# Performance work log

Measured on AMD Instinct MI355X. Metric: run time of the kernel, lower is better.

Reference implementation:

```python
import jax, jax.numpy as jnp
import numpy as np
from jax import lax

B, C_IN, C_OUT, K, STYLE_DIM, H, W = 16, 128, 128, 3, 512, 128, 128
EPS = 1e-8


def setup_inputs() -> dict:
    key = jax.random.key(0)
    k1, k2, k3, k4 = jax.random.split(key, 4)
    x = jax.random.normal(k1, (B, C_IN, H, W), dtype=jnp.float32)
    style_vector = jax.random.normal(k2, (B, STYLE_DIM), dtype=jnp.float32)
    # EqualizedLR(nn.Linear(style_dim, in_channels)): weight ~ N(0,1), bias = 0
    proj_w = jax.random.normal(k3, (C_IN, STYLE_DIM), dtype=jnp.float32)
    proj_b = jnp.zeros((C_IN,), dtype=jnp.float32)
    # base conv weight (1, out, in, k, k) ~ N(0,1)
    weight = jax.random.normal(k4, (1, C_OUT, C_IN, K, K), dtype=jnp.float32)
    return {"x": x, "style_vector": style_vector, "proj_w": proj_w,
            "proj_b": proj_b, "weight": weight}


def reference(x, style_vector, proj_w, proj_b, weight):
    b = x.shape[0]
    # EqualizedLR: scale input by gain / sqrt(fan_in), gain=1, fan_in=style_dim
    scale = 1.0 / jnp.sqrt(jnp.float32(STYLE_DIM))
    style = (style_vector * scale) @ proj_w.T + proj_b          # [b, in]
    # modulate: [1,out,in,k,k] * [b,1,in,1,1] -> [b,out,in,k,k]
    w = weight * style[:, None, :, None, None]
    # demodulate
    demod = lax.rsqrt(jnp.sum(w * w, axis=(2, 3, 4)) + EPS)     # [b, out]
    w = w * demod[:, :, None, None, None]
    # grouped conv with groups=b == per-sample conv; vmap over batch
    pad = K // 2
    def conv_one(xi, wi):
        # xi: [in,H,W], wi: [out,in,k,k]
        return lax.conv_general_dilated(
            xi[None], wi, window_strides=(1, 1),
            padding=[(pad, pad), (pad, pad)],
            dimension_numbers=("NCHW", "OIHW", "NCHW"))[0]
    out = jax.vmap(conv_one)(x, w)                               # [b,out,H,W]
    return out
```

## Files before the change

kernel.cpp:

```cpp
#include <hip/hip_runtime.h>
#include <cstdint>

#define B_   16
#define CIN  128
#define COUT 128
#define SD   512
#define H_   128
#define W_   128

typedef __bf16 bf16x8  __attribute__((ext_vector_type(8)));
typedef float  floatx4 __attribute__((ext_vector_type(4)));
typedef float floatx16 __attribute__((ext_vector_type(16)));

__global__ void style_kernel(const float* __restrict__ sv, const float* __restrict__ pw,
                             const float* __restrict__ pb, float* __restrict__ style) {
    int bid = blockIdx.x;
    int b = bid >> 7, c = bid & 127;
    int lane = threadIdx.x;
    const float* svb = sv + b * SD;
    const float* pwc = pw + (size_t)c * SD;
    float s = 0.f;
#pragma unroll
    for (int i = 0; i < SD; i += 64) s += svb[i + lane] * pwc[i + lane];
#pragma unroll
    for (int off = 32; off > 0; off >>= 1) s += __shfl_down(s, off, 64);
    if (lane == 0) style[b * CIN + c] = s * 0.044194173824159216f + pb[c];
}

__global__ void modw_kernel(const float* __restrict__ weight, const float* __restrict__ style,
                            __bf16* __restrict__ wmod) {
    int bid = blockIdx.x;
    int b = bid >> 7, o = bid & 127;
    int c = threadIdx.x;
    float s = style[b * CIN + c];
    const float* wp = weight + ((size_t)o * CIN + c) * 9;
    float v[9];
    float ss = 0.f;
#pragma unroll
    for (int t = 0; t < 9; ++t) { v[t] = wp[t] * s; ss += v[t] * v[t]; }
#pragma unroll
    for (int off = 32; off > 0; off >>= 1) ss += __shfl_down(ss, off, 64);
    __shared__ float sh[2];
    int wid = c >> 6, lane = c & 63;
    if (lane == 0) sh[wid] = ss;
    __syncthreads();
    float d = rsqrtf(sh[0] + sh[1] + 1e-8f);
    int chunk = c >> 4, ci = c & 15;
#pragma unroll
    for (int t = 0; t < 9; ++t) {
        wmod[(((((size_t)b * 9 + t) * 8 + chunk) * 128 + o) * 16 + ci)] = (__bf16)(v[t] * d);
    }
}

__global__ __launch_bounds__(256)
void xpose_kernel(const float* __restrict__ x, __bf16* __restrict__ xT) {
    int ch = blockIdx.x;
    int hq = blockIdx.y;
    int b  = blockIdx.z;
    int t  = threadIdx.x;
    int wq = t & 31;
    int cp = t >> 5;
    int c0 = ch * 16 + cp * 2;
    const float* xa = x + (((size_t)b * CIN + c0    ) * H_ + hq * 8) * W_ + wq * 4;
    const float* xc = x + (((size_t)b * CIN + c0 + 1) * H_ + hq * 8) * W_ + wq * 4;
    uint32_t* dst = (uint32_t*)xT + ((((size_t)b * 8 + ch) * H_ + hq * 8) * W_) * 8 + cp;
#pragma unroll
    for (int hr = 0; hr < 8; ++hr) {
        floatx4 a  = *(const floatx4*)(xa + (size_t)hr * W_);
        floatx4 b2 = *(const floatx4*)(xc + (size_t)hr * W_);
#pragma unroll
        for (int j = 0; j < 4; ++j) {
            unsigned short lo = __builtin_bit_cast(unsigned short, (__bf16)a[j]);
            unsigned short hi = __builtin_bit_cast(unsigned short, (__bf16)b2[j]);
            dst[(size_t)hr * W_ * 8 + (size_t)(wq * 4 + j) * 8] =
                (uint32_t)lo | ((uint32_t)hi << 16);
        }
    }
}

#define WXT 66
__global__ __launch_bounds__(256, 4)
void conv_kernel(const __bf16* __restrict__ xT, const __bf16* __restrict__ wmod,
                 float* __restrict__ out) {
    __shared__ __align__(16) __bf16 Xs[4 * WXT * 16];
    int w0 = blockIdx.x * 64;
    int h0 = blockIdx.y * 2;
    int b  = blockIdx.z;
    int tid = threadIdx.x;
    int wv = tid >> 6, lane = tid & 63;
    int n = lane & 31, hf = lane >> 5;
    int obase = (wv & 1) * 64;
    int r = wv >> 1;

    floatx16 acc[2][2];
#pragma unroll
    for (int i = 0; i < 2; ++i)
#pragma unroll
        for (int j = 0; j < 2; ++j)
#pragma unroll
            for (int k = 0; k < 16; ++k) acc[i][j][k] = 0.f;

    const __bf16* xb = xT + (size_t)b * 8 * H_ * W_ * 16;

    for (int ch = 0; ch < 8; ++ch) {
        __syncthreads();
        for (int idx = tid; idx < 4 * WXT * 2; idx += 256) {
            int row = idx / (WXT * 2);
            int rem = idx - row * (WXT * 2);
            int wp = rem >> 1, g = rem & 1;
            int hh = h0 - 1 + row, ww = w0 - 1 + wp;
            bf16x8 v;
#pragma unroll
            for (int k = 0; k < 8; ++k) v[k] = (__bf16)0.f;
            if ((unsigned)hh < (unsigned)H_ && (unsigned)ww < (unsigned)W_)
                v = *(const bf16x8*)(xb + ((((size_t)ch * H_ + hh) * W_ + ww) * 16) + g * 8);
            *(bf16x8*)(&Xs[(size_t)idx * 8]) = v;
        }
        __syncthreads();

#pragma unroll
        for (int tap = 0; tap < 9; ++tap) {
            int kh = tap / 3, kw = tap % 3;
            const __bf16* ap = wmod +
                (((((size_t)b * 9 + tap) * 8 + ch) * 128 + obase + n) * 16 + hf * 8);
            bf16x8 a0 = *(const bf16x8*)ap;
            bf16x8 a1 = *(const bf16x8*)(ap + 32 * 16);
            int row = r + kh;
#pragma unroll
            for (int wt = 0; wt < 2; ++wt) {
                int wp = wt * 32 + n + kw;
                bf16x8 bfrag = *(const bf16x8*)(&Xs[(row * WXT + wp) * 16 + hf * 8]);
                acc[0][wt] = __builtin_amdgcn_mfma_f32_32x32x16_bf16(a0, bfrag, acc[0][wt], 0, 0, 0);
                acc[1][wt] = __builtin_amdgcn_mfma_f32_32x32x16_bf16(a1, bfrag, acc[1][wt], 0, 0, 0);
            }
        }
    }

    float* ob = out + (((size_t)b * COUT) * H_ + (h0 + r)) * W_ + w0;
#pragma unroll
    for (int i = 0; i < 2; ++i) {
#pragma unroll
        for (int reg = 0; reg < 16; ++reg) {
            int o = obase + i * 32 + (reg & 3) + 8 * (reg >> 2) + 4 * hf;
#pragma unroll
            for (int wt = 0; wt < 2; ++wt)
                ob[(size_t)o * (H_ * W_) + wt * 32 + n] = acc[i][wt][reg];
        }
    }
}

extern "C" void kernel_launch(void* const* d_in, const int* in_sizes, int n_in,
                              void* d_out, int out_size, void* d_ws, size_t ws_size,
                              hipStream_t stream) {
    const float* x      = (const float*)d_in[0];
    const float* sv     = (const float*)d_in[1];
    const float* pw     = (const float*)d_in[2];
    const float* pb     = (const float*)d_in[3];
    const float* weight = (const float*)d_in[4];
    float* out = (float*)d_out;

    float*  style = (float*)d_ws;
    __bf16* wmod  = (__bf16*)((char*)d_ws + 8192);
    __bf16* xT    = (__bf16*)((char*)d_ws + 8192 + 4718592);

    style_kernel<<<B_ * CIN, 64, 0, stream>>>(sv, pw, pb, style);
    modw_kernel<<<B_ * COUT, 128, 0, stream>>>(weight, style, wmod);
    xpose_kernel<<<dim3(8, 16, B_), 256, 0, stream>>>(x, xT);
    conv_kernel<<<dim3(2, 64, B_), 256, 0, stream>>>(xT, wmod, out);
}
```

Measured before the change: 344.5 us.

## Double-buffer conv input tile, prefetch weights, and LDS-stage the transpose

```diff
diff --git a/kernel.cpp b/kernel.cpp
--- a/kernel.cpp
+++ b/kernel.cpp
@@ -54,35 +54,48 @@
 
 __global__ __launch_bounds__(256)
 void xpose_kernel(const float* __restrict__ x, __bf16* __restrict__ xT) {
+    __shared__ uint32_t T[4 * 4 * 8 * 32];
     int ch = blockIdx.x;
     int hq = blockIdx.y;
     int b  = blockIdx.z;
     int t  = threadIdx.x;
+    int cp = t >> 5;
     int wq = t & 31;
-    int cp = t >> 5;
     int c0 = ch * 16 + cp * 2;
-    const float* xa = x + (((size_t)b * CIN + c0    ) * H_ + hq * 8) * W_ + wq * 4;
-    const float* xc = x + (((size_t)b * CIN + c0 + 1) * H_ + hq * 8) * W_ + wq * 4;
-    uint32_t* dst = (uint32_t*)xT + ((((size_t)b * 8 + ch) * H_ + hq * 8) * W_) * 8 + cp;
-#pragma unroll
-    for (int hr = 0; hr < 8; ++hr) {
-        floatx4 a  = *(const floatx4*)(xa + (size_t)hr * W_);
-        floatx4 b2 = *(const floatx4*)(xc + (size_t)hr * W_);
+    const float* pa = x + (((size_t)b * CIN + c0    ) * H_ + hq * 4) * W_ + wq * 4;
+    const float* pc = x + (((size_t)b * CIN + c0 + 1) * H_ + hq * 4) * W_ + wq * 4;
+#pragma unroll
+    for (int hr = 0; hr < 4; ++hr) {
+        floatx4 va = *(const floatx4*)(pa + (size_t)hr * W_);
+        floatx4 vb = *(const floatx4*)(pc + (size_t)hr * W_);
 #pragma unroll
         for (int j = 0; j < 4; ++j) {
-            unsigned short lo = __builtin_bit_cast(unsigned short, (__bf16)a[j]);
-            unsigned short hi = __builtin_bit_cast(unsigned short, (__bf16)b2[j]);
-            dst[(size_t)hr * W_ * 8 + (size_t)(wq * 4 + j) * 8] =
-                (uint32_t)lo | ((uint32_t)hi << 16);
-        }
+            uint32_t lo = (uint32_t)__builtin_bit_cast(unsigned short, (__bf16)va[j]);
+            uint32_t hi = (uint32_t)__builtin_bit_cast(unsigned short, (__bf16)vb[j]);
+            T[((hr * 4 + j) * 8 + cp) * 32 + wq] = lo | (hi << 16);
+        }
+    }
+    __syncthreads();
+    uint32_t* dst = (uint32_t*)xT + ((((size_t)b * 8 + ch) * H_ + hq * 4) * W_) * 8;
+#pragma unroll
+    for (int it = 0; it < 8; ++it) {
+        int o0 = it * 512 + t * 2;
+        int cpr = o0 & 7;
+        int w   = (o0 >> 3) & 127;
+        int hr  = o0 >> 10;
+        int base = ((hr * 4 + (w & 3)) * 8);
+        uint32_t v0 = T[(base + cpr    ) * 32 + (w >> 2)];
+        uint32_t v1 = T[(base + cpr + 1) * 32 + (w >> 2)];
+        uint2 pk; pk.x = v0; pk.y = v1;
+        *(uint2*)(dst + o0) = pk;
     }
 }
 
 #define WXT 66
-__global__ __launch_bounds__(256, 4)
+__global__ __launch_bounds__(256, 2)
 void conv_kernel(const __bf16* __restrict__ xT, const __bf16* __restrict__ wmod,
                  float* __restrict__ out) {
-    __shared__ __align__(16) __bf16 Xs[4 * WXT * 16];
+    __shared__ __align__(16) __bf16 Xs[2][4 * WXT * 16];
     int w0 = blockIdx.x * 64;
     int h0 = blockIdx.y * 2;
     int b  = blockIdx.z;
@@ -102,36 +115,64 @@
 
     const __bf16* xb = xT + (size_t)b * 8 * H_ * W_ * 16;
 
+    bool sact[3], sval[3];
+    const __bf16* sptr[3];
+    int soff[3];
+#pragma unroll
+    for (int s = 0; s < 3; ++s) {
+        int idx = tid + s * 256;
+        bool act = (s < 2) || (tid < 16);
+        int row = idx / 132;
+        int rem = idx - row * 132;
+        int wp = rem >> 1, g = rem & 1;
+        int hh = h0 - 1 + row, ww = w0 - 1 + wp;
+        sact[s] = act;
+        sval[s] = act && (unsigned)hh < (unsigned)H_ && (unsigned)ww < (unsigned)W_;
+        sptr[s] = xb + ((size_t)hh * W_ + ww) * 16 + g * 8;
+        soff[s] = idx * 8;
+    }
+
+    bf16x8 sv[3];
+#pragma unroll
+    for (int s = 0; s < 3; ++s) {
+#pragma unroll
+        for (int k = 0; k < 8; ++k) sv[s][k] = (__bf16)0.f;
+        if (sval[s]) sv[s] = *(const bf16x8*)(sptr[s]);
+    }
+
+    const __bf16* apb = wmod + ((((size_t)b * 9) * 8) * 128 + obase + n) * 16 + hf * 8;
+
     for (int ch = 0; ch < 8; ++ch) {
+        bf16x8 a[9][2];
+#pragma unroll
+        for (int tap = 0; tap < 9; ++tap) {
+            const __bf16* ap = apb + tap * 16384 + ch * 2048;
+            a[tap][0] = *(const bf16x8*)ap;
+            a[tap][1] = *(const bf16x8*)(ap + 512);
+        }
+        __bf16* xbuf = Xs[ch & 1];
+#pragma unroll
+        for (int s = 0; s < 3; ++s)
+            if (sact[s]) *(bf16x8*)(xbuf + soff[s]) = sv[s];
+        if (ch < 7) {
+#pragma unroll
+            for (int s = 0; s < 3; ++s) {
+#pragma unroll
+                for (int k = 0; k < 8; ++k) sv[s][k] = (__bf16)0.f;
+                if (sval[s]) sv[s] = *(const bf16x8*)(sptr[s] + (size_t)(ch + 1) * (H_ * W_ * 16));
+            }
+        }
         __syncthreads();
-        for (int idx = tid; idx < 4 * WXT * 2; idx += 256) {
-            int row = idx / (WXT * 2);
-            int rem = idx - row * (WXT * 2);
-            int wp = rem >> 1, g = rem & 1;
-            int hh = h0 - 1 + row, ww = w0 - 1 + wp;
-            bf16x8 v;
-#pragma unroll
-            for (int k = 0; k < 8; ++k) v[k] = (__bf16)0.f;
-            if ((unsigned)hh < (unsigned)H_ && (unsigned)ww < (unsigned)W_)
-                v = *(const bf16x8*)(xb + ((((size_t)ch * H_ + hh) * W_ + ww) * 16) + g * 8);
-            *(bf16x8*)(&Xs[(size_t)idx * 8]) = v;
-        }
-        __syncthreads();
-
 #pragma unroll
         for (int tap = 0; tap < 9; ++tap) {
             int kh = tap / 3, kw = tap % 3;
-            const __bf16* ap = wmod +
-                (((((size_t)b * 9 + tap) * 8 + ch) * 128 + obase + n) * 16 + hf * 8);
-            bf16x8 a0 = *(const bf16x8*)ap;
-            bf16x8 a1 = *(const bf16x8*)(ap + 32 * 16);
             int row = r + kh;
 #pragma unroll
             for (int wt = 0; wt < 2; ++wt) {
                 int wp = wt * 32 + n + kw;
-                bf16x8 bfrag = *(const bf16x8*)(&Xs[(row * WXT + wp) * 16 + hf * 8]);
-                acc[0][wt] = __builtin_amdgcn_mfma_f32_32x32x16_bf16(a0, bfrag, acc[0][wt], 0, 0, 0);
-                acc[1][wt] = __builtin_amdgcn_mfma_f32_32x32x16_bf16(a1, bfrag, acc[1][wt], 0, 0, 0);
+                bf16x8 bfrag = *(const bf16x8*)(xbuf + (row * WXT + wp) * 16 + hf * 8);
+                acc[0][wt] = __builtin_amdgcn_mfma_f32_32x32x16_bf16(a[tap][0], bfrag, acc[0][wt], 0, 0, 0);
+                acc[1][wt] = __builtin_amdgcn_mfma_f32_32x32x16_bf16(a[tap][1], bfrag, acc[1][wt], 0, 0, 0);
             }
         }
     }
@@ -144,7 +185,8 @@
             int o = obase + i * 32 + (reg & 3) + 8 * (reg >> 2) + 4 * hf;
 #pragma unroll
             for (int wt = 0; wt < 2; ++wt)
-                ob[(size_t)o * (H_ * W_) + wt * 32 + n] = acc[i][wt][reg];
+                __builtin_nontemporal_store(acc[i][wt][reg],
+                    &ob[(size_t)o * (H_ * W_) + wt * 32 + n]);
         }
     }
 }
@@ -165,6 +207,6 @@
 
     style_kernel<<<B_ * CIN, 64, 0, stream>>>(sv, pw, pb, style);
     modw_kernel<<<B_ * COUT, 128, 0, stream>>>(weight, style, wmod);
-    xpose_kernel<<<dim3(8, 16, B_), 256, 0, stream>>>(x, xT);
+    xpose_kernel<<<dim3(8, 32, B_), 256, 0, stream>>>(x, xT);
     conv_kernel<<<dim3(2, 64, B_), 256, 0, stream>>>(xT, wmod, out);
 }
```

Result: faster. 308.9 us (-10.3%).
